# Kernel tuning notes

Measured on AMD Instinct MI355X. Metric: run time of the kernel, lower is better.

## Reference

```python
import jax, jax.numpy as jnp
import numpy as np

YOLO_INPUT_SIZE = 416.0
SCORE_THRESHOLD = 0.5
IOU_THRESHOLD = 0.45
AREA_THRESHOLD = 0.0005
MAX_OUTPUT_BOXES = 10
NEG = -1e9


def setup_inputs() -> dict:
    key = jax.random.key(0)
    y = jax.random.uniform(key, (64, 10647, 85), dtype=jnp.float32)
    # first 4 channels are xywh in input-pixel units (YOLO decode divides by 416)
    y = y.at[..., 0:2].multiply(YOLO_INPUT_SIZE)          # centers in [0, 416)
    y = y.at[..., 2:4].multiply(YOLO_INPUT_SIZE * 0.3)    # w,h up to ~125 px
    return {"y_pred": y}


def _decode(y_pred):
    flat = y_pred.reshape(-1, y_pred.shape[-1])           # [N, 85]
    box, conf, probs = flat[:, :4], flat[:, 4], flat[:, 5:]
    scores = conf * jnp.max(probs, axis=-1)               # [N]
    classes = jnp.argmax(probs, axis=-1).astype(jnp.int32)
    b = jnp.clip(box / YOLO_INPUT_SIZE, 0.0, 1.0)
    x, y, w, h = b[:, 0], b[:, 1], b[:, 2], b[:, 3]
    x1 = jnp.clip(x - w * 0.5, 0.0, 1.0)
    y1 = jnp.clip(y - h * 0.5, 0.0, 1.0)
    x2 = jnp.clip(x + w * 0.5, 0.0, 1.0)
    y2 = jnp.clip(y + h * 0.5, 0.0, 1.0)
    big_enough = (x2 - x1) * (y2 - y1) > AREA_THRESHOLD
    keep = big_enough & (scores > SCORE_THRESHOLD)
    boxes = jnp.stack([x1, y1, x2, y2], axis=-1)          # [N, 4]
    work = jnp.where(keep, scores, NEG)                   # masked working scores
    return boxes, scores, classes, work


def _iou_one_vs_all(ref, boxes):
    ix1 = jnp.maximum(ref[0], boxes[:, 0])
    iy1 = jnp.maximum(ref[1], boxes[:, 1])
    ix2 = jnp.minimum(ref[2], boxes[:, 2])
    iy2 = jnp.minimum(ref[3], boxes[:, 3])
    inter = jnp.maximum(ix2 - ix1, 0.0) * jnp.maximum(iy2 - iy1, 0.0)
    a_ref = (ref[2] - ref[0]) * (ref[3] - ref[1])
    a_all = (boxes[:, 2] - boxes[:, 0]) * (boxes[:, 3] - boxes[:, 1])
    return inter / (a_ref + a_all - inter + 1e-10)


def _greedy_nms(boxes, work):
    def step(w, _):
        j = jnp.argmax(w)
        v = w[j] > SCORE_THRESHOLD
        iou = _iou_one_vs_all(boxes[j], boxes)
        w = jnp.where(v & (iou > IOU_THRESHOLD), NEG, w)
        w = w.at[j].set(NEG)
        return w, (j.astype(jnp.int32), v)
    _, (idxs, valid) = jax.lax.scan(step, work, None, length=MAX_OUTPUT_BOXES)
    return idxs, valid


def reference(y_pred):
    boxes, scores, classes, work = _decode(y_pred)
    idxs, valid = _greedy_nms(boxes, work)
    # fixed-size (padded) outputs instead of dynamic boolean gather; `valid`
    # marks real detections (original returns only the valid rows)
    sel_boxes = boxes[idxs]                # [10, 4]
    sel_scores = scores[idxs][:, None]     # [10, 1]
    sel_classes = classes[idxs][:, None]   # [10, 1]
    return sel_boxes, sel_scores, sel_classes, valid
```

## Files before the change

### kernel.cpp

```cpp
#include <hip/hip_runtime.h>

#define ROWS   681408
#define NBINS  8192
#define CAP    64
#define TOPK   192
#define SELCAP 256

#define WS_ROW0     4
#define WS_CNT      16
#define WS_BUCKET   8448

__device__ __forceinline__ float clip01(float v) {
    return fminf(fmaxf(v, 0.0f), 1.0f);
}

__global__ void init_kernel(unsigned int* __restrict__ ws) {
    int i = blockIdx.x * 256 + threadIdx.x;
    if (i < NBINS) ws[WS_CNT + i] = 0u;
}

__global__ __launch_bounds__(256) void decode_kernel(
    const float* __restrict__ y, unsigned int* __restrict__ ws)
{
    const int t    = threadIdx.x;
    const int lane = t & 63;
    const int wave = t >> 6;
    const int g    = lane >> 4;
    const int s    = lane & 15;
    const int row  = blockIdx.x * 16 + wave * 4 + g;

    const float* p = y + (size_t)row * 85;

    float e0 = (s < 8) ? p[s] : -1.0f;

    const int gb = lane & 48;
    float cf = __shfl(e0, gb + 4, 64);

    bool gate = (cf > 0.5f) || (row == 0);
    if (!gate) return;

    if (s >= 8) e0 = p[s];
    float e1 = p[s + 16];
    float e2 = p[s + 32];
    float e3 = p[s + 48];
    float e4 = p[s + 64];
    float e5 = (s < 5) ? p[s + 80] : -1.0f;

    float bv; int bc;
    if (s >= 5) { bv = e0; bc = s - 5; } else { bv = -1.0f; bc = 1 << 20; }
    if (e1 > bv) { bv = e1; bc = s + 11; }
    if (e2 > bv) { bv = e2; bc = s + 27; }
    if (e3 > bv) { bv = e3; bc = s + 43; }
    if (e4 > bv) { bv = e4; bc = s + 59; }
    if (s < 5 && e5 > bv) { bv = e5; bc = s + 75; }

    #pragma unroll
    for (int m = 8; m >= 1; m >>= 1) {
        float ov = __shfl_xor(bv, m, 64);
        int   oc = __shfl_xor(bc, m, 64);
        if (ov > bv || (ov == bv && oc < bc)) { bv = ov; bc = oc; }
    }

    float bx = __shfl(e0, gb + 0, 64);
    float by = __shfl(e0, gb + 1, 64);
    float bw = __shfl(e0, gb + 2, 64);
    float bh = __shfl(e0, gb + 3, 64);

    if (s == 0) {
        float score = cf * bv;
        float x  = clip01(bx / 416.0f);
        float yy = clip01(by / 416.0f);
        float w  = clip01(bw / 416.0f);
        float h  = clip01(bh / 416.0f);
        float x1 = clip01(x  - w * 0.5f);
        float y1 = clip01(yy - h * 0.5f);
        float x2 = clip01(x  + w * 0.5f);
        float y2 = clip01(yy + h * 0.5f);
        bool keep = (((x2 - x1) * (y2 - y1)) > 0.0005f) && (score > 0.5f);
        if (keep) {
            int bin = (int)((score - 0.5f) * (2.0f * (float)NBINS));
            bin = min(max(bin, 0), NBINS - 1);
            unsigned int pos = atomicAdd(&ws[WS_CNT + bin], 1u);
            if (pos < (unsigned int)CAP) {
                uint2* bucket = (uint2*)&ws[WS_BUCKET];
                bucket[bin * CAP + pos] =
                    make_uint2(__float_as_uint(score), (unsigned int)row);
            }
        }
        if (row == 0) {
            float* r0 = (float*)&ws[WS_ROW0];
            r0[0] = score; r0[1] = (float)bc;
            r0[2] = x1; r0[3] = y1; r0[4] = x2; r0[5] = y2;
        }
    }
}

__global__ __launch_bounds__(256) void nms_kernel(
    const float* __restrict__ y, unsigned int* __restrict__ ws,
    float* __restrict__ out)
{
    __shared__ unsigned int chunk[256];
    __shared__ unsigned long long keys[SELCAP];
    __shared__ float4 sboxes[SELCAP];
    __shared__ int s_bstar;
    __shared__ unsigned int s_m;
    __shared__ int s_picks;
    __shared__ unsigned int s_idx[10];
    __shared__ float s_score[10];
    __shared__ float4 s_box[10];
    __shared__ int s_cls[10];

    const int t = threadIdx.x;
    const uint2* bucket = (const uint2*)&ws[WS_BUCKET];

    unsigned int ssum = 0;
    {
        const uint4* cnt4 = (const uint4*)&ws[WS_CNT];
        #pragma unroll
        for (int i = 0; i < 8; i++) {
            uint4 v = cnt4[t * 8 + i];
            ssum += min(v.x, (unsigned int)CAP) + min(v.y, (unsigned int)CAP)
                  + min(v.z, (unsigned int)CAP) + min(v.w, (unsigned int)CAP);
        }
    }
    chunk[t] = ssum;
    for (int i = t; i < SELCAP; i += 256) keys[i] = 0ull;
    __syncthreads();
    if (t == 0) {
        unsigned int total = 0;
        for (int c = 0; c < 256; c++) total += chunk[c];
        unsigned int target = (total < (unsigned int)TOPK) ? total : (unsigned int)TOPK;
        int b = NBINS;
        if (target > 0) {
            unsigned int cum = 0;
            int c;
            for (c = 255; c >= 0; c--) {
                if (cum + chunk[c] >= target) break;
                cum += chunk[c];
            }
            if (c < 0) {
                b = 0;
            } else {
                int bb;
                for (bb = c * 32 + 31; bb >= c * 32; bb--) {
                    unsigned int cc = ws[WS_CNT + bb];
                    cum += (cc < (unsigned int)CAP) ? cc : (unsigned int)CAP;
                    if (cum >= target) break;
                }
                b = max(bb, c * 32);
            }
        }
        s_bstar = b;
        s_m = 0u;
    }
    __syncthreads();

    for (int bin = s_bstar + t; bin < NBINS; bin += 256) {
        unsigned int c = ws[WS_CNT + bin];
        if (c > (unsigned int)CAP) c = CAP;
        for (unsigned int j = 0; j < c; j++) {
            uint2 cv = bucket[bin * CAP + j];
            unsigned int pos = atomicAdd(&s_m, 1u);
            if (pos < (unsigned int)SELCAP)
                keys[pos] = ((unsigned long long)cv.x << 32) |
                            (unsigned long long)(0xFFFFFFFFu - cv.y);
        }
    }
    __syncthreads();
    unsigned int M = s_m;
    if (M > (unsigned int)SELCAP) M = SELCAP;

    for (int k = 2; k <= SELCAP; k <<= 1) {
        for (int j = k >> 1; j > 0; j >>= 1) {
            for (int i = t; i < SELCAP; i += 256) {
                int ixj = i ^ j;
                if (ixj > i) {
                    unsigned long long a = keys[i], b = keys[ixj];
                    bool descSeg = ((i & k) == 0);
                    if (descSeg ? (a < b) : (a > b)) { keys[i] = b; keys[ixj] = a; }
                }
            }
            __syncthreads();
        }
    }

    for (int i = t; i < (int)M; i += 256) {
        unsigned int idx = 0xFFFFFFFFu - (unsigned int)(keys[i] & 0xFFFFFFFFull);
        const float* p = y + (size_t)idx * 85;
        float x  = clip01(p[0] / 416.0f);
        float yy = clip01(p[1] / 416.0f);
        float w  = clip01(p[2] / 416.0f);
        float h  = clip01(p[3] / 416.0f);
        sboxes[i] = make_float4(clip01(x - w * 0.5f), clip01(yy - h * 0.5f),
                                clip01(x + w * 0.5f), clip01(yy + h * 0.5f));
    }
    __syncthreads();

    if (t == 0) {
        int np = 0;
        for (int i = 0; i < (int)M && np < 10; i++) {
            float4 b = sboxes[i];
            bool ok = true;
            for (int kk = 0; kk < np; kk++) {
                float4 r = s_box[kk];
                float ix1 = fmaxf(r.x, b.x);
                float iy1 = fmaxf(r.y, b.y);
                float ix2 = fminf(r.z, b.z);
                float iy2 = fminf(r.w, b.w);
                float inter = fmaxf(ix2 - ix1, 0.0f) * fmaxf(iy2 - iy1, 0.0f);
                float aref = (r.z - r.x) * (r.w - r.y);
                float aall = (b.z - b.x) * (b.w - b.y);
                float iou = inter / (aref + aall - inter + 1e-10f);
                if (iou > 0.45f) { ok = false; break; }
            }
            if (ok) {
                s_box[np] = b;
                s_idx[np] = 0xFFFFFFFFu - (unsigned int)(keys[i] & 0xFFFFFFFFull);
                s_score[np] = __uint_as_float((unsigned int)(keys[i] >> 32));
                np++;
            }
        }
        s_picks = np;
    }
    __syncthreads();

    {
        int p = t >> 4, s = t & 15;
        float bv = -1.0f; int bc = 1 << 20;
        if (p < s_picks) {
            const float* pr = y + (size_t)s_idx[p] * 85 + 5;
            #pragma unroll
            for (int kk = 0; kk < 5; kk++) {
                float v = pr[s + 16 * kk];
                int c = s + 16 * kk;
                if (v > bv) { bv = v; bc = c; }
            }
        }
        #pragma unroll
        for (int m = 8; m >= 1; m >>= 1) {
            float ov = __shfl_xor(bv, m, 64);
            int   oc = __shfl_xor(bc, m, 64);
            if (ov > bv || (ov == bv && oc < bc)) { bv = ov; bc = oc; }
        }
        if (p < s_picks && s == 0) s_cls[p] = bc;
    }
    __syncthreads();

    if (t == 0) {
        const float* r0 = (const float*)&ws[WS_ROW0];
        float score0 = r0[0], class0 = r0[1];
        float4 box0 = make_float4(r0[2], r0[3], r0[4], r0[5]);
        for (int kk = 0; kk < 10; kk++) {
            bool v = kk < s_picks;
            float4 b = v ? s_box[kk] : box0;
            out[4 * kk + 0] = b.x;
            out[4 * kk + 1] = b.y;
            out[4 * kk + 2] = b.z;
            out[4 * kk + 3] = b.w;
            out[40 + kk] = v ? s_score[kk] : score0;
            out[50 + kk] = v ? (float)s_cls[kk] : class0;
            out[60 + kk] = v ? 1.0f : 0.0f;
        }
    }
}

extern "C" void kernel_launch(void* const* d_in, const int* in_sizes, int n_in,
                              void* d_out, int out_size, void* d_ws, size_t ws_size,
                              hipStream_t stream)
{
    const float* y = (const float*)d_in[0];
    unsigned int* ws = (unsigned int*)d_ws;

    init_kernel<<<dim3(NBINS / 256), dim3(256), 0, stream>>>(ws);
    decode_kernel<<<dim3(ROWS / 16), dim3(256), 0, stream>>>(y, ws);
    nms_kernel<<<dim3(1), dim3(256), 0, stream>>>(y, ws, (float*)d_out);
}
```

Baseline: 81.12 us.

## Vectorize decode row loads and parallelize NMS threshold-bin search with suffix scans

The decode kernel now reads each 85-float row as float2 pairs in one pass, replacing the confidence-gated two-phase load, and takes coordinates and confidence from shuffled pair values. Because every row is now loaded in full, the early exit that skipped rows with confidence at or below 0.5 is gone. The NMS kernel's single-threaded serial search for the cutoff bin is replaced by parallel Hillis-Steele suffix scans over the 256 coarse chunks and then the 32 fine bins. The scans add many block barriers, and the decode kernel now moves more memory traffic.

```diff
diff --git a/kernel.cpp b/kernel.cpp
--- a/kernel.cpp
+++ b/kernel.cpp
@@ -29,30 +29,25 @@
     const int s    = lane & 15;
     const int row  = blockIdx.x * 16 + wave * 4 + g;
 
-    const float* p = y + (size_t)row * 85;
-
-    float e0 = (s < 8) ? p[s] : -1.0f;
-
-    const int gb = lane & 48;
-    float cf = __shfl(e0, gb + 4, 64);
-
-    bool gate = (cf > 0.5f) || (row == 0);
-    if (!gate) return;
-
-    if (s >= 8) e0 = p[s];
-    float e1 = p[s + 16];
-    float e2 = p[s + 32];
-    float e3 = p[s + 48];
-    float e4 = p[s + 64];
-    float e5 = (s < 5) ? p[s + 80] : -1.0f;
-
-    float bv; int bc;
-    if (s >= 5) { bv = e0; bc = s - 5; } else { bv = -1.0f; bc = 1 << 20; }
-    if (e1 > bv) { bv = e1; bc = s + 11; }
-    if (e2 > bv) { bv = e2; bc = s + 27; }
-    if (e3 > bv) { bv = e3; bc = s + 43; }
-    if (e4 > bv) { bv = e4; bc = s + 59; }
-    if (s < 5 && e5 > bv) { bv = e5; bc = s + 75; }
+    const float*  p  = y + (size_t)row * 85;
+    const float2* p2 = (const float2*)p;
+
+    float2 A = p2[s];
+    float2 B = p2[s + 16];
+    float c0 = -1.0f, c1 = -1.0f;
+    if (s < 10) { float2 C = p2[s + 32]; c0 = C.x; c1 = C.y; }
+    else if (s == 10) { c0 = p[84]; }
+
+    float bv = -1.0f; int bc = 1 << 20;
+    {
+        int e = 2 * s;
+        if (e >= 5 && A.x > bv) { bv = A.x; bc = e - 5; }
+        if (e + 1 >= 5 && A.y > bv) { bv = A.y; bc = e - 4; }
+        if (B.x > bv) { bv = B.x; bc = e + 27; }
+        if (B.y > bv) { bv = B.y; bc = e + 28; }
+        if (e + 64 <= 84 && c0 > bv) { bv = c0; bc = e + 59; }
+        if (e + 65 <= 84 && c1 > bv) { bv = c1; bc = e + 60; }
+    }
 
     #pragma unroll
     for (int m = 8; m >= 1; m >>= 1) {
@@ -61,10 +56,12 @@
         if (ov > bv || (ov == bv && oc < bc)) { bv = ov; bc = oc; }
     }
 
-    float bx = __shfl(e0, gb + 0, 64);
-    float by = __shfl(e0, gb + 1, 64);
-    float bw = __shfl(e0, gb + 2, 64);
-    float bh = __shfl(e0, gb + 3, 64);
+    const int gb = lane & 48;
+    float bx = __shfl(A.x, gb + 0, 64);
+    float by = __shfl(A.y, gb + 0, 64);
+    float bw = __shfl(A.x, gb + 1, 64);
+    float bh = __shfl(A.y, gb + 1, 64);
+    float cf = __shfl(A.x, gb + 2, 64);
 
     if (s == 0) {
         float score = cf * bv;
@@ -100,8 +97,10 @@
     float* __restrict__ out)
 {
     __shared__ unsigned int chunk[256];
+    __shared__ unsigned int fine[32];
     __shared__ unsigned long long keys[SELCAP];
     __shared__ float4 sboxes[SELCAP];
+    __shared__ int s_coarse;
     __shared__ int s_bstar;
     __shared__ unsigned int s_m;
     __shared__ int s_picks;
@@ -125,33 +124,43 @@
     }
     chunk[t] = ssum;
     for (int i = t; i < SELCAP; i += 256) keys[i] = 0ull;
-    __syncthreads();
-    if (t == 0) {
-        unsigned int total = 0;
-        for (int c = 0; c < 256; c++) total += chunk[c];
-        unsigned int target = (total < (unsigned int)TOPK) ? total : (unsigned int)TOPK;
-        int b = NBINS;
-        if (target > 0) {
-            unsigned int cum = 0;
-            int c;
-            for (c = 255; c >= 0; c--) {
-                if (cum + chunk[c] >= target) break;
-                cum += chunk[c];
-            }
-            if (c < 0) {
-                b = 0;
-            } else {
-                int bb;
-                for (bb = c * 32 + 31; bb >= c * 32; bb--) {
-                    unsigned int cc = ws[WS_CNT + bb];
-                    cum += (cc < (unsigned int)CAP) ? cc : (unsigned int)CAP;
-                    if (cum >= target) break;
-                }
-                b = max(bb, c * 32);
-            }
-        }
-        s_bstar = b;
-        s_m = 0u;
+    if (t == 0) s_m = 0u;
+    __syncthreads();
+
+    for (int off = 1; off < 256; off <<= 1) {
+        unsigned int v = chunk[t];
+        unsigned int a = (t + off < 256) ? chunk[t + off] : 0u;
+        __syncthreads();
+        chunk[t] = v + a;
+        __syncthreads();
+    }
+    const unsigned int total  = chunk[0];
+    const unsigned int target = (total < (unsigned int)TOPK) ? total
+                                                             : (unsigned int)TOPK;
+
+    if (target > 0) {
+        if (chunk[t] >= target && (t == 255 || chunk[t + 1] < target))
+            s_coarse = t;
+        __syncthreads();
+
+        const int cb = s_coarse * 32;
+        if (t < 32) fine[t] = min(ws[WS_CNT + cb + t], (unsigned int)CAP);
+        __syncthreads();
+        for (int off = 1; off < 32; off <<= 1) {
+            unsigned int v = 0, a = 0;
+            if (t < 32) { v = fine[t]; a = (t + off < 32) ? fine[t + off] : 0u; }
+            __syncthreads();
+            if (t < 32) fine[t] = v + a;
+            __syncthreads();
+        }
+        const unsigned int base = (s_coarse < 255) ? chunk[s_coarse + 1] : 0u;
+        if (t < 32) {
+            unsigned int sfx = base + fine[t];
+            unsigned int nxt = (t == 31) ? base : base + fine[t + 1];
+            if (sfx >= target && nxt < target) s_bstar = cb + t;
+        }
+    } else {
+        if (t == 0) s_bstar = NBINS;
     }
     __syncthreads();
 
```

New measurement: 78.09 us. -3.7%, faster.
